# Optimization experiments

Hardware: AMD Instinct MI355X
Metric: run time of the kernel (lower is better)

Reference implementation:

```python
import jax, jax.numpy as jnp
import numpy as np

N, NFEAT, NHID, NCLASS, NHEADS = 4096, 512, 64, 16, 8
ALPHA = 0.2  # LeakyReLU negative slope


def setup_inputs() -> dict:
    key = jax.random.key(0)
    ks = jax.random.split(key, 5)
    return {
        "x": jax.random.normal(ks[0], (N, NFEAT), jnp.float32),
        "Wh": jax.random.normal(ks[1], (NHEADS, NFEAT, NHID), jnp.float32) * 0.05,
        "ah": jax.random.normal(ks[2], (NHEADS, 2 * NHID), jnp.float32) * 0.1,
        "Wo": jax.random.normal(ks[3], (NHEADS * NHID, NCLASS), jnp.float32) * 0.05,
        "ao": jax.random.normal(ks[4], (2 * NCLASS,), jnp.float32) * 0.1,
    }


def _gat_layer(x, W, a, concat):
    # h = x W  [N, F]
    h = x @ W
    F = h.shape[-1]
    # additive score decomposes: e_ij = leakyrelu(h_i . a[:F] + h_j . a[F:])
    s_src = h @ a[:F]  # [N]
    s_dst = h @ a[F:]  # [N]
    e = jax.nn.leaky_relu(s_src[:, None] + s_dst[None, :], ALPHA)  # [N, N]
    att = jax.nn.softmax(e, axis=1)
    feat = att @ h  # [N, F]
    return jax.nn.elu(feat) if concat else feat


def reference(x, Wh, ah, Wo, ao):
    # multi-head layers, concatenated along features (head-major order, as torch cat)
    heads = jax.vmap(lambda W, a: _gat_layer(x, W, a, True))(Wh, ah)  # [H, N, nhid]
    xc = jnp.transpose(heads, (1, 0, 2)).reshape(x.shape[0], -1)  # [N, H*nhid]
    out = jax.nn.elu(_gat_layer(xc, Wo, ao, False))  # [N, nclass]
    return jax.nn.log_softmax(out, axis=1)
```

## Files before the change

### kernel.cpp

```cpp
#include <hip/hip_runtime.h>
#include <math.h>

#define N 4096
#define NFEAT 512
#define NHID 64
#define NCLASS 16
#define NHEADS 8
#define ALPHA 0.2f
#define NC 256
#define JSPL 8
#define JLEN (N / JSPL)
#define HSTR 520

typedef __attribute__((ext_vector_type(8))) short bf16x8;
typedef __attribute__((ext_vector_type(4))) float f32x4;

__device__ inline unsigned short f2bf(float f) {
  unsigned u = __float_as_uint(f);
  unsigned r = u + 0x7fffu + ((u >> 16) & 1u);
  return (unsigned short)(r >> 16);
}
__device__ inline float bf2f(unsigned short u) {
  return __uint_as_float(((unsigned)u) << 16);
}
__device__ inline unsigned mono(float f) {
  unsigned u = __float_as_uint(f);
  return (u & 0x80000000u) ? ~u : (u | 0x80000000u);
}
__device__ inline float unmono(unsigned m) {
  return (m >> 31) ? __uint_as_float(m & 0x7FFFFFFFu) : __uint_as_float(~m);
}

__global__ __launch_bounds__(256) void k_pack(const float* __restrict__ x,
                                              const float* __restrict__ Wh,
                                              const float* __restrict__ Wo,
                                              unsigned short* __restrict__ xb,
                                              unsigned short* __restrict__ Wt,
                                              unsigned short* __restrict__ Wt2,
                                              unsigned* __restrict__ tmax2u) {
  int b = blockIdx.x;
  if (b < 2048) {
    int i = (b * 256 + threadIdx.x) * 4;
    float4 v = *(const float4*)(x + i);
    ushort4 o;
    o.x = f2bf(v.x); o.y = f2bf(v.y); o.z = f2bf(v.z); o.w = f2bf(v.w);
    *(ushort4*)(xb + i) = o;
  } else if (b < 2112) {
    int idx = b - 2048;
    int kt = idx & 7, hd = idx >> 3;
    __shared__ float ld[64][65];
    const float* src = Wh + ((size_t)hd * NFEAT + kt * 64) * NHID;
    int r = threadIdx.x >> 2, c0 = (threadIdx.x & 3) * 16;
#pragma unroll
    for (int j = 0; j < 4; ++j) {
      float4 v = *(const float4*)(src + (size_t)r * NHID + c0 + j * 4);
      ld[r][c0 + j * 4 + 0] = v.x; ld[r][c0 + j * 4 + 1] = v.y;
      ld[r][c0 + j * 4 + 2] = v.z; ld[r][c0 + j * 4 + 3] = v.w;
    }
    __syncthreads();
    int n = threadIdx.x >> 2, kq = threadIdx.x & 3;
    unsigned short tmp[16];
#pragma unroll
    for (int j = 0; j < 16; ++j) tmp[j] = f2bf(ld[kq * 16 + j][n]);
    unsigned short* dst = Wt + ((size_t)hd * 64 + n) * NFEAT + kt * 64 + kq * 16;
    ((uint4*)dst)[0] = *(uint4*)tmp;
    ((uint4*)dst)[1] = *(uint4*)(tmp + 8);
  } else {
    for (int e = threadIdx.x; e < NFEAT * NCLASS; e += 256) {
      int n = e & 15, k = e >> 4;
      Wt2[(size_t)n * NFEAT + k] = f2bf(Wo[(size_t)k * NCLASS + n]);
    }
    if (threadIdx.x == 0) *tmax2u = 0u;
  }
}

__global__ __launch_bounds__(256) void k_gemm_h(const unsigned short* __restrict__ xb,
                                                const unsigned short* __restrict__ Wt,
                                                const float* __restrict__ ah,
                                                unsigned short* __restrict__ h1b,
                                                float* __restrict__ ssrc,
                                                float* __restrict__ sdst) {
  const int hd = blockIdx.y;
  const int i0 = blockIdx.x * 128;
  const int t = threadIdx.x;
  const int w = t >> 6, lane = t & 63;
  const int lr = lane & 15, kg = lane >> 4;
  const int wm = (w & 1) * 64, wn = (w >> 1) * 32;
  __shared__ uint4 Als[128][4];
  __shared__ uint4 Bls[64][4];
  __shared__ float sredS[128][2];
  __shared__ float sredD[128][2];
  const unsigned short* xrow = xb + (size_t)i0 * NFEAT;
  const unsigned short* wrow = Wt + (size_t)hd * 64 * NFEAT;

  f32x4 acc[4][2];
#pragma unroll
  for (int a = 0; a < 4; ++a)
#pragma unroll
    for (int b = 0; b < 2; ++b) acc[a][b] = (f32x4){0.f, 0.f, 0.f, 0.f};

  const int u0 = t, u1 = t + 256;
  const int ra0 = u0 >> 2, sa0 = ((u0 & 3) ^ (ra0 & 3)) * 8;
  const int ra1 = u1 >> 2, sa1 = ((u1 & 3) ^ (ra1 & 3)) * 8;
  const int rb0 = t >> 2,  sb0 = ((t & 3) ^ (rb0 & 3)) * 8;
  const int wbase = t & ~63;

  for (int k0 = 0; k0 < NFEAT; k0 += 32) {
    __builtin_amdgcn_global_load_lds(
        (const __attribute__((address_space(1))) void*)(xrow + (size_t)ra0 * NFEAT + k0 + sa0),
        (__attribute__((address_space(3))) void*)((uint4*)Als + wbase), 16, 0, 0);
    __builtin_amdgcn_global_load_lds(
        (const __attribute__((address_space(1))) void*)(xrow + (size_t)ra1 * NFEAT + k0 + sa1),
        (__attribute__((address_space(3))) void*)((uint4*)Als + 256 + wbase), 16, 0, 0);
    __builtin_amdgcn_global_load_lds(
        (const __attribute__((address_space(1))) void*)(wrow + (size_t)rb0 * NFEAT + k0 + sb0),
        (__attribute__((address_space(3))) void*)((uint4*)Bls + wbase), 16, 0, 0);
    __syncthreads();
    bf16x8 af[4], bfv[2];
#pragma unroll
    for (int mb = 0; mb < 4; ++mb) {
      int row = wm + mb * 16 + lr;
      af[mb] = __builtin_bit_cast(bf16x8, Als[row][kg ^ (row & 3)]);
    }
#pragma unroll
    for (int nb = 0; nb < 2; ++nb) {
      int col = wn + nb * 16 + lr;
      bfv[nb] = __builtin_bit_cast(bf16x8, Bls[col][kg ^ (col & 3)]);
    }
#pragma unroll
    for (int mb = 0; mb < 4; ++mb)
#pragma unroll
      for (int nb = 0; nb < 2; ++nb)
        acc[mb][nb] = __builtin_amdgcn_mfma_f32_16x16x32_bf16(af[mb], bfv[nb], acc[mb][nb], 0, 0, 0);
    __syncthreads();
  }

  unsigned short* hout = h1b + ((size_t)hd * N + i0) * NHID;
#pragma unroll
  for (int mb = 0; mb < 4; ++mb)
#pragma unroll
    for (int nb = 0; nb < 2; ++nb) {
      int rbase = wm + mb * 16 + kg * 4;
      int col = wn + nb * 16 + lr;
#pragma unroll
      for (int reg = 0; reg < 4; ++reg)
        hout[(size_t)(rbase + reg) * NHID + col] = f2bf(acc[mb][nb][reg]);
    }

  float aS[2], aD[2];
#pragma unroll
  for (int nb = 0; nb < 2; ++nb) {
    aS[nb] = ah[hd * 128 + wn + nb * 16 + lr];
    aD[nb] = ah[hd * 128 + 64 + wn + nb * 16 + lr];
  }
#pragma unroll
  for (int mb = 0; mb < 4; ++mb)
#pragma unroll
    for (int reg = 0; reg < 4; ++reg) {
      float ps = acc[mb][0][reg] * aS[0] + acc[mb][1][reg] * aS[1];
      float pd = acc[mb][0][reg] * aD[0] + acc[mb][1][reg] * aD[1];
#pragma unroll
      for (int m = 1; m < 16; m <<= 1) { ps += __shfl_xor(ps, m); pd += __shfl_xor(pd, m); }
      if (lr == 0) {
        int rl = wm + mb * 16 + kg * 4 + reg;
        sredS[rl][w >> 1] = ps;
        sredD[rl][w >> 1] = pd;
      }
    }
  __syncthreads();
  if (t < 128) {
    ssrc[(size_t)hd * N + i0 + t] = sredS[t][0] + sredS[t][1];
    sdst[(size_t)hd * N + i0 + t] = sredD[t][0] + sredD[t][1];
  }
}

__global__ __launch_bounds__(256) void k_rank(const float* __restrict__ t,
                                              const float* __restrict__ ssrc,
                                              float* __restrict__ ts,
                                              int* __restrict__ perm,
                                              int* __restrict__ ksp) {
  int hd = blockIdx.y;
  const float* th = t + (size_t)hd * N;
  __shared__ unsigned skey[N];
  int tid = threadIdx.x;
  for (int i = tid; i < N; i += 256)
    skey[i] = (mono(th[i]) & 0xFFFFF000u) | (unsigned)i;
  __syncthreads();
  int wv = tid >> 6, lane = tid & 63;
  int jbase = blockIdx.x * 64 + wv * 16;
  unsigned kj[16], qk[16];
  int cnt[16], cq[16];
#pragma unroll
  for (int jj = 0; jj < 16; ++jj) {
    kj[jj] = skey[jbase + jj];
    qk[jj] = (mono(-ssrc[(size_t)hd * N + jbase + jj]) & 0xFFFFF000u) | 0xFFFu;
    cnt[jj] = 0; cq[jj] = 0;
  }
  for (int c = 0; c < N; c += 64) {
    unsigned key = skey[c + lane];
#pragma unroll
    for (int jj = 0; jj < 16; ++jj) {
      cnt[jj] += __popcll(__ballot(key < kj[jj]));
      cq[jj]  += __popcll(__ballot(key < qk[jj]));
    }
  }
  int myc = 0, myq = 0;
#pragma unroll
  for (int jj = 0; jj < 16; ++jj)
    if (lane == jj) { myc = cnt[jj]; myq = cq[jj]; }
  if (lane < 16) {
    int j = jbase + lane;
    ts[(size_t)hd * N + myc] = th[j];
    perm[(size_t)hd * N + myc] = j;
    ksp[(size_t)hd * N + j] = myq;
  }
}

__global__ __launch_bounds__(256) void k_chunksum1(const float* __restrict__ ts,
                                                   const int* __restrict__ perm,
                                                   const unsigned short* __restrict__ h1b,
                                                   float* __restrict__ csA,
                                                   float* __restrict__ csB,
                                                   float* __restrict__ csAz,
                                                   float* __restrict__ csBz) {
  int hd = blockIdx.y, lane = threadIdx.x & 63;
  int c = blockIdx.x * 4 + (threadIdx.x >> 6);
  int r0 = c * 16;
  float tm = ts[(size_t)hd * N + N - 1];
  float tvv = ts[(size_t)hd * N + r0 + (lane & 15)];
  float ev = expf((lane < 16 ? ALPHA : 1.f) * (tvv - tm));
  int pvv = perm[(size_t)hd * N + r0 + (lane & 15)];
  float sA = 0.f, sB = 0.f, zA = 0.f, zB = 0.f;
#pragma unroll
  for (int r = 0; r < 16; ++r) {
    float eA = __shfl(ev, r);
    float eB = __shfl(ev, 16 + r);
    int p = __shfl(pvv, r);
    float hv = bf2f(h1b[((size_t)hd * N + p) * NHID + lane]);
    sA += eA * hv; sB += eB * hv; zA += eA; zB += eB;
  }
  csA[((size_t)hd * NC + c) * NHID + lane] = sA;
  csB[((size_t)hd * NC + c) * NHID + lane] = sB;
  if (lane == 0) { csAz[hd * NC + c] = zA; csBz[hd * NC + c] = zB; }
}

__global__ __launch_bounds__(1024) void k_chunkscan1(float* __restrict__ csA,
                                                     float* __restrict__ csB,
                                                     float* __restrict__ csAz,
                                                     float* __restrict__ csBz) {
  int hd = blockIdx.x;
  int t = threadIdx.x, w = t >> 6, lane = t & 63;
  __shared__ float pA[16][64], pB[16][64];
  __shared__ float pAz[16], pBz[16];
  float rA[16], rB[16], rAz[16], rBz[16];
#pragma unroll
  for (int cc = 0; cc < 16; ++cc) {
    int c = w * 16 + cc;
    rA[cc] = csA[((size_t)hd * NC + c) * NHID + lane];
    rB[cc] = csB[((size_t)hd * NC + c) * NHID + lane];
    rAz[cc] = csAz[hd * NC + c];
    rBz[cc] = csBz[hd * NC + c];
  }
  float tA = 0.f, tB = 0.f, tAz = 0.f, tBz = 0.f;
#pragma unroll
  for (int cc = 0; cc < 16; ++cc) { tA += rA[cc]; tB += rB[cc]; tAz += rAz[cc]; tBz += rBz[cc]; }
  pA[w][lane] = tA; pB[w][lane] = tB;
  if (lane == 0) { pAz[w] = tAz; pBz[w] = tBz; }
  __syncthreads();
  float bA = 0.f, bAz = 0.f, bB = 0.f, bBz = 0.f;
  for (int w2 = 0; w2 < w; ++w2) { bA += pA[w2][lane]; bAz += pAz[w2]; }
  for (int w2 = w + 1; w2 < 16; ++w2) { bB += pB[w2][lane]; bBz += pBz[w2]; }
  float run = bA, runz = bAz;
#pragma unroll
  for (int cc = 0; cc < 16; ++cc) {
    int c = w * 16 + cc;
    csA[((size_t)hd * NC + c) * NHID + lane] = run; run += rA[cc];
    if (lane == 0) csAz[hd * NC + c] = runz;
    runz += rAz[cc];
  }
  run = bB; runz = bBz;
#pragma unroll
  for (int cc = 15; cc >= 0; --cc) {
    int c = w * 16 + cc;
    csB[((size_t)hd * NC + c) * NHID + lane] = run; run += rB[cc];
    if (lane == 0) csBz[hd * NC + c] = runz;
    runz += rBz[cc];
  }
}

__global__ __launch_bounds__(256) void k_combine1(const float* __restrict__ ssrc,
                                                  const float* __restrict__ ts,
                                                  const int* __restrict__ perm,
                                                  const int* __restrict__ ksp,
                                                  const unsigned short* __restrict__ h1b,
                                                  const float* __restrict__ csA,
                                                  const float* __restrict__ csB,
                                                  const float* __restrict__ csAz,
                                                  const float* __restrict__ csBz,
                                                  unsigned short* __restrict__ xcb) {
  int hd = blockIdx.x >> 8;
  int base = (blockIdx.x & 255) * 16;
  int w = threadIdx.x >> 6, lane = threadIdx.x & 63;
  const float* tsh = ts + (size_t)hd * N;
  float tm = tsh[N - 1];
  for (int it = 0; it < 4; ++it) {
    int i = base + w * 4 + it;
    float s = ssrc[(size_t)hd * N + i];
    int k = ksp[(size_t)hd * N + i];
    int c = k >> 4; if (c > NC - 1) c = NC - 1;
    int c0 = c * 16;
    float v = s + tm;
    float m = fmaxf(v, ALPHA * v);
    float wA = expf(ALPHA * v - m), wB = expf(v - m);
    size_t cb = (size_t)hd * NC + c;
    float numA = csA[cb * NHID + lane];
    float numB = csB[cb * NHID + lane];
    float zA = csAz[cb], zB = csBz[cb];
    int r15 = lane & 15;
    float tvv = tsh[c0 + r15];
    int pvv = perm[(size_t)hd * N + c0 + r15];
    float ev = expf(((c0 + r15) < k ? ALPHA : 1.f) * (tvv - tm));
#pragma unroll
    for (int r = 0; r < 16; ++r) {
      float e = __shfl(ev, r);
      int p = __shfl(pvv, r);
      float hv = bf2f(h1b[((size_t)hd * N + p) * NHID + lane]);
      bool isA = (c0 + r) < k;
      if (isA) { numA += e * hv; zA += e; } else { numB += e * hv; zB += e; }
    }
    float Z = wA * zA + wB * zB;
    float f = (wA * numA + wB * numB) / Z;
    float e2 = f > 0.f ? f : expf(f) - 1.f;
    xcb[(size_t)i * (NHEADS * NHID) + hd * NHID + lane] = f2bf(e2);
  }
}

__global__ __launch_bounds__(256) void k_gemm2(const unsigned short* __restrict__ xcb,
                                               const unsigned short* __restrict__ Wt2,
                                               const float* __restrict__ ao,
                                               unsigned short* __restrict__ h2b,
                                               float* __restrict__ ssrc,
                                               float* __restrict__ sdst,
                                               unsigned* __restrict__ tmax2u) {
  const int t = threadIdx.x;
  const int w = t >> 6, lane = t & 63;
  const int lr = lane & 15, kg = lane >> 4;
  const int i0 = blockIdx.x * 64 + w * 16;
  __shared__ float sd[64];
  f32x4 acc = (f32x4){0.f, 0.f, 0.f, 0.f};
  const unsigned short* arow = xcb + (size_t)(i0 + lr) * NFEAT;
  const unsigned short* brow = Wt2 + (size_t)lr * NFEAT;
#pragma unroll
  for (int k0 = 0; k0 < NFEAT; k0 += 32) {
    bf16x8 af = __builtin_bit_cast(bf16x8, *(const uint4*)(arow + k0 + kg * 8));
    bf16x8 bv = __builtin_bit_cast(bf16x8, *(const uint4*)(brow + k0 + kg * 8));
    acc = __builtin_amdgcn_mfma_f32_16x16x32_bf16(af, bv, acc, 0, 0, 0);
  }
  float aS = ao[lr], aD = ao[16 + lr];
#pragma unroll
  for (int reg = 0; reg < 4; ++reg) {
    int row = i0 + kg * 4 + reg;
    h2b[(size_t)row * NCLASS + lr] = f2bf(acc[reg]);
    float ps = acc[reg] * aS, pd = acc[reg] * aD;
#pragma unroll
    for (int m = 1; m < 16; m <<= 1) { ps += __shfl_xor(ps, m); pd += __shfl_xor(pd, m); }
    if (lr == 0) {
      ssrc[row] = ps;
      sdst[row] = pd;
      sd[w * 16 + kg * 4 + reg] = pd;
    }
  }
  __syncthreads();
  if (t < 64) {
    float v = sd[t];
#pragma unroll
    for (int m = 32; m; m >>= 1) v = fmaxf(v, __shfl_xor(v, m));
    if (t == 0) atomicMax(tmax2u, mono(v));
  }
}

__global__ __launch_bounds__(256) void k_attn2p(const float* __restrict__ ssrc,
                                                const float* __restrict__ t,
                                                const unsigned short* __restrict__ h2b,
                                                const unsigned* __restrict__ tmax2u,
                                                float* __restrict__ pnum,
                                                float* __restrict__ pz) {
  __shared__ float tl[JLEN];
  __shared__ unsigned short hsT[16 * HSTR];
  int tid = threadIdx.x;
  int jb = blockIdx.y;
  if (tid < 128) {
    int i4 = tid * 4;
    *(float4*)(tl + i4) = *(const float4*)(t + jb * JLEN + i4);
  }
#pragma unroll
  for (int rep = 0; rep < 2; ++rep) {
    int j = rep * 256 + tid;
    const uint4* src = (const uint4*)(h2b + (size_t)(jb * JLEN + j) * NCLASS);
    uint4 a = src[0], b = src[1];
    unsigned short v[16];
    *(uint4*)v = a; *(uint4*)(v + 8) = b;
#pragma unroll
    for (int c = 0; c < 16; ++c) hsT[c * HSTR + j] = v[c];
  }
  __syncthreads();
  int w = tid >> 6, lane = tid & 63;
  int lr = lane & 15, kg = lane >> 4;
  int ib = blockIdx.x * 64 + w * 16;
  float tmax = unmono(*tmax2u);
  float s = ssrc[ib + lr];
  float v0 = s + tmax;
  float rowm = fmaxf(v0, ALPHA * v0);
  f32x4 acc = (f32x4){0.f, 0.f, 0.f, 0.f};
  float zpart = 0.f;
#pragma unroll
  for (int c = 0; c < JLEN / 32; ++c) {
    const float* tp = tl + c * 32 + kg * 8;
    float e[8];
#pragma unroll
    for (int m = 0; m < 8; ++m) {
      float v = s + tp[m];
      e[m] = __expf(fmaxf(v, ALPHA * v) - rowm);
      zpart += e[m];
    }
    unsigned pk[4];
#pragma unroll
    for (int p = 0; p < 4; ++p)
      pk[p] = ((unsigned)f2bf(e[2 * p + 1]) << 16) | (unsigned)f2bf(e[2 * p]);
    bf16x8 af = __builtin_bit_cast(bf16x8, *(uint4*)pk);
    bf16x8 bf = __builtin_bit_cast(bf16x8,
        *(const uint4*)(hsT + lr * HSTR + c * 32 + kg * 8));
    acc = __builtin_amdgcn_mfma_f32_16x16x32_bf16(af, bf, acc, 0, 0, 0);
  }
  zpart += __shfl_xor(zpart, 16);
  zpart += __shfl_xor(zpart, 32);
#pragma unroll
  for (int reg = 0; reg < 4; ++reg)
    pnum[((size_t)jb * N + ib + kg * 4 + reg) * NCLASS + lr] = acc[reg];
  if (lane < 16) pz[(size_t)jb * N + ib + lane] = zpart;
}

__global__ __launch_bounds__(256) void k_attn2f(const float* __restrict__ pnum,
                                                const float* __restrict__ pz,
                                                float* __restrict__ out) {
  int g = threadIdx.x >> 4, cl = threadIdx.x & 15;
  int i = blockIdx.x * 16 + g;
  float nsum = 0.f, zsum = 0.f;
#pragma unroll
  for (int jb = 0; jb < JSPL; ++jb) {
    nsum += pnum[((size_t)jb * N + i) * NCLASS + cl];
    zsum += pz[(size_t)jb * N + i];
  }
  float o = nsum / zsum;
  o = o > 0.f ? o : expf(o) - 1.f;
  float mo = o;
#pragma unroll
  for (int mk = 1; mk < 16; mk <<= 1) mo = fmaxf(mo, __shfl_xor(mo, mk, 16));
  float sum = expf(o - mo);
#pragma unroll
  for (int mk = 1; mk < 16; mk <<= 1) sum += __shfl_xor(sum, mk, 16);
  out[(size_t)i * NCLASS + cl] = o - mo - logf(sum);
}

extern "C" void kernel_launch(void* const* d_in, const int* in_sizes, int n_in,
                              void* d_out, int out_size, void* d_ws, size_t ws_size,
                              hipStream_t stream) {
  const float* x  = (const float*)d_in[0];
  const float* Wh = (const float*)d_in[1];
  const float* ah = (const float*)d_in[2];
  const float* Wo = (const float*)d_in[3];
  const float* ao = (const float*)d_in[4];
  float* out = (float*)d_out;

  char* base = (char*)d_ws;
  size_t off = 0;
  auto alloc_f = [&](size_t n) -> float* {
    float* p = (float*)(base + off);
    off = (off + n * sizeof(float) + 255) & ~(size_t)255;
    return p;
  };
  auto alloc_i = [&](size_t n) -> int* {
    int* p = (int*)(base + off);
    off = (off + n * sizeof(int) + 255) & ~(size_t)255;
    return p;
  };
  auto alloc_u16 = [&](size_t n) -> unsigned short* {
    unsigned short* p = (unsigned short*)(base + off);
    off = (off + n * sizeof(unsigned short) + 255) & ~(size_t)255;
    return p;
  };

  unsigned short* xbf = alloc_u16((size_t)N * NFEAT);
  unsigned short* Wt  = alloc_u16((size_t)NHEADS * NHID * NFEAT);
  unsigned short* Wt2 = alloc_u16((size_t)NCLASS * NFEAT);
  unsigned short* h1b = alloc_u16((size_t)NHEADS * N * NHID);
  float* ssrc1 = alloc_f((size_t)NHEADS * N);
  float* sdst1 = alloc_f((size_t)NHEADS * N);
  float* ts1   = alloc_f((size_t)NHEADS * N);
  int*   perm1 = alloc_i((size_t)NHEADS * N);
  int*   ksp1  = alloc_i((size_t)NHEADS * N);
  float* csA1  = alloc_f((size_t)NHEADS * NC * NHID);
  float* csB1  = alloc_f((size_t)NHEADS * NC * NHID);
  float* csAz1 = alloc_f(NHEADS * NC);
  float* csBz1 = alloc_f(NHEADS * NC);
  unsigned short* xcb = alloc_u16((size_t)N * NHEADS * NHID);
  unsigned short* h2b = alloc_u16((size_t)N * NCLASS);
  float* ssrc2 = alloc_f(N);
  float* sdst2 = alloc_f(N);
  unsigned* tmax2u = (unsigned*)alloc_i(1);
  float* pnum  = alloc_f((size_t)JSPL * N * NCLASS);
  float* pz    = alloc_f((size_t)JSPL * N);

  if (off > ws_size) return;

  hipLaunchKernelGGL(k_pack, dim3(2113), dim3(256), 0, stream, x, Wh, Wo, xbf, Wt, Wt2, tmax2u);

  hipLaunchKernelGGL(k_gemm_h, dim3(N / 128, NHEADS), dim3(256), 0, stream, xbf, Wt, ah, h1b, ssrc1, sdst1);
  hipLaunchKernelGGL(k_rank, dim3(64, NHEADS), dim3(256), 0, stream, sdst1, ssrc1, ts1, perm1, ksp1);
  hipLaunchKernelGGL(k_chunksum1, dim3(64, NHEADS), dim3(256), 0, stream, ts1, perm1, h1b, csA1, csB1, csAz1, csBz1);
  hipLaunchKernelGGL(k_chunkscan1, dim3(NHEADS), dim3(1024), 0, stream, csA1, csB1, csAz1, csBz1);
  hipLaunchKernelGGL(k_combine1, dim3(NHEADS * 256), dim3(256), 0, stream, ssrc1, ts1, perm1, ksp1, h1b, csA1, csB1, csAz1, csBz1, xcb);

  hipLaunchKernelGGL(k_gemm2, dim3(N / 64), dim3(256), 0, stream, xcb, Wt2, ao, h2b, ssrc2, sdst2, tmax2u);
  hipLaunchKernelGGL(k_attn2p, dim3(N / 64, JSPL), dim3(256), 0, stream, ssrc2, sdst2, h2b, tmax2u, pnum, pz);
  hipLaunchKernelGGL(k_attn2f, dim3(N / 16), dim3(256), 0, stream, pnum, pz, out);
}
```

Before: 105.7 us.

## Replace sort-based layer-1 attention with dense MFMA attention over transposed h

Drops the rank/sort, chunk-sum, chunk-scan and combine pipeline for the first GAT layer. In its place is a single dense attention kernel: it uses a per-head global max of the destination scores (found with atomicMax in the projection GEMM) as the softmax shift, builds exp weights as bf16 and multiplies them against h with MFMA. h is now stored transposed so tiles stage into LDS with contiguous loads. This cuts four launches and the gather-heavy sorted traversal, but the attention becomes O(N^2·F) matrix work per head and the exp weights are rounded to bf16.

After: 106.0 us. About the same (+0.3%).

```diff
diff --git a/kernel.cpp b/kernel.cpp
--- a/kernel.cpp
+++ b/kernel.cpp
@@ -7,10 +7,11 @@
 #define NCLASS 16
 #define NHEADS 8
 #define ALPHA 0.2f
-#define NC 256
 #define JSPL 8
 #define JLEN (N / JSPL)
 #define HSTR 520
+#define J1 256
+#define H1STR 264
 
 typedef __attribute__((ext_vector_type(8))) short bf16x8;
 typedef __attribute__((ext_vector_type(4))) float f32x4;
@@ -19,9 +20,6 @@
   unsigned u = __float_as_uint(f);
   unsigned r = u + 0x7fffu + ((u >> 16) & 1u);
   return (unsigned short)(r >> 16);
-}
-__device__ inline float bf2f(unsigned short u) {
-  return __uint_as_float(((unsigned)u) << 16);
 }
 __device__ inline unsigned mono(float f) {
   unsigned u = __float_as_uint(f);
@@ -37,6 +35,7 @@
                                               unsigned short* __restrict__ xb,
                                               unsigned short* __restrict__ Wt,
                                               unsigned short* __restrict__ Wt2,
+                                              unsigned* __restrict__ tmax1u,
                                               unsigned* __restrict__ tmax2u) {
   int b = blockIdx.x;
   if (b < 2048) {
@@ -70,6 +69,7 @@
       int n = e & 15, k = e >> 4;
       Wt2[(size_t)n * NFEAT + k] = f2bf(Wo[(size_t)k * NCLASS + n]);
     }
+    if (threadIdx.x < NHEADS) tmax1u[threadIdx.x] = 0u;
     if (threadIdx.x == 0) *tmax2u = 0u;
   }
 }
@@ -77,9 +77,10 @@
 __global__ __launch_bounds__(256) void k_gemm_h(const unsigned short* __restrict__ xb,
                                                 const unsigned short* __restrict__ Wt,
                                                 const float* __restrict__ ah,
-                                                unsigned short* __restrict__ h1b,
+                                                unsigned short* __restrict__ h1T,
                                                 float* __restrict__ ssrc,
-                                                float* __restrict__ sdst) {
+                                                float* __restrict__ sdst,
+                                                unsigned* __restrict__ tmax1u) {
   const int hd = blockIdx.y;
   const int i0 = blockIdx.x * 128;
   const int t = threadIdx.x;
@@ -135,16 +136,17 @@
     __syncthreads();
   }
 
-  unsigned short* hout = h1b + ((size_t)hd * N + i0) * NHID;
+  unsigned short* hT = h1T + (size_t)hd * NHID * N;
 #pragma unroll
   for (int mb = 0; mb < 4; ++mb)
 #pragma unroll
     for (int nb = 0; nb < 2; ++nb) {
-      int rbase = wm + mb * 16 + kg * 4;
       int col = wn + nb * 16 + lr;
-#pragma unroll
-      for (int reg = 0; reg < 4; ++reg)
-        hout[(size_t)(rbase + reg) * NHID + col] = f2bf(acc[mb][nb][reg]);
+      int rbase = i0 + wm + mb * 16 + kg * 4;
+      ushort4 o;
+      o.x = f2bf(acc[mb][nb][0]); o.y = f2bf(acc[mb][nb][1]);
+      o.z = f2bf(acc[mb][nb][2]); o.w = f2bf(acc[mb][nb][3]);
+      *(ushort4*)(hT + (size_t)col * N + rbase) = o;
     }
 
   float aS[2], aD[2];
@@ -169,169 +171,85 @@
     }
   __syncthreads();
   if (t < 128) {
-    ssrc[(size_t)hd * N + i0 + t] = sredS[t][0] + sredS[t][1];
-    sdst[(size_t)hd * N + i0 + t] = sredD[t][0] + sredD[t][1];
-  }
-}
-
-__global__ __launch_bounds__(256) void k_rank(const float* __restrict__ t,
-                                              const float* __restrict__ ssrc,
-                                              float* __restrict__ ts,
-                                              int* __restrict__ perm,
-                                              int* __restrict__ ksp) {
-  int hd = blockIdx.y;
-  const float* th = t + (size_t)hd * N;
-  __shared__ unsigned skey[N];
-  int tid = threadIdx.x;
-  for (int i = tid; i < N; i += 256)
-    skey[i] = (mono(th[i]) & 0xFFFFF000u) | (unsigned)i;
-  __syncthreads();
-  int wv = tid >> 6, lane = tid & 63;
-  int jbase = blockIdx.x * 64 + wv * 16;
-  unsigned kj[16], qk[16];
-  int cnt[16], cq[16];
-#pragma unroll
-  for (int jj = 0; jj < 16; ++jj) {
-    kj[jj] = skey[jbase + jj];
-    qk[jj] = (mono(-ssrc[(size_t)hd * N + jbase + jj]) & 0xFFFFF000u) | 0xFFFu;
-    cnt[jj] = 0; cq[jj] = 0;
-  }
-  for (int c = 0; c < N; c += 64) {
-    unsigned key = skey[c + lane];
-#pragma unroll
-    for (int jj = 0; jj < 16; ++jj) {
-      cnt[jj] += __popcll(__ballot(key < kj[jj]));
-      cq[jj]  += __popcll(__ballot(key < qk[jj]));
-    }
-  }
-  int myc = 0, myq = 0;
-#pragma unroll
-  for (int jj = 0; jj < 16; ++jj)
-    if (lane == jj) { myc = cnt[jj]; myq = cq[jj]; }
-  if (lane < 16) {
-    int j = jbase + lane;
-    ts[(size_t)hd * N + myc] = th[j];
-    perm[(size_t)hd * N + myc] = j;
-    ksp[(size_t)hd * N + j] = myq;
-  }
-}
-
-__global__ __launch_bounds__(256) void k_chunksum1(const float* __restrict__ ts,
-                                                   const int* __restrict__ perm,
-                                                   const unsigned short* __restrict__ h1b,
-                                                   float* __restrict__ csA,
-                                                   float* __restrict__ csB,
-                                                   float* __restrict__ csAz,
-                                                   float* __restrict__ csBz) {
-  int hd = blockIdx.y, lane = threadIdx.x & 63;
-  int c = blockIdx.x * 4 + (threadIdx.x >> 6);
-  int r0 = c * 16;
-  float tm = ts[(size_t)hd * N + N - 1];
-  float tvv = ts[(size_t)hd * N + r0 + (lane & 15)];
-  float ev = expf((lane < 16 ? ALPHA : 1.f) * (tvv - tm));
-  int pvv = perm[(size_t)hd * N + r0 + (lane & 15)];
-  float sA = 0.f, sB = 0.f, zA = 0.f, zB = 0.f;
-#pragma unroll
-  for (int r = 0; r < 16; ++r) {
-    float eA = __shfl(ev, r);
-    float eB = __shfl(ev, 16 + r);
-    int p = __shfl(pvv, r);
-    float hv = bf2f(h1b[((size_t)hd * N + p) * NHID + lane]);
-    sA += eA * hv; sB += eB * hv; zA += eA; zB += eB;
-  }
-  csA[((size_t)hd * NC + c) * NHID + lane] = sA;
-  csB[((size_t)hd * NC + c) * NHID + lane] = sB;
-  if (lane == 0) { csAz[hd * NC + c] = zA; csBz[hd * NC + c] = zB; }
-}
-
-__global__ __launch_bounds__(1024) void k_chunkscan1(float* __restrict__ csA,
-                                                     float* __restrict__ csB,
-                                                     float* __restrict__ csAz,
-                                                     float* __restrict__ csBz) {
-  int hd = blockIdx.x;
-  int t = threadIdx.x, w = t >> 6, lane = t & 63;
-  __shared__ float pA[16][64], pB[16][64];
-  __shared__ float pAz[16], pBz[16];
-  float rA[16], rB[16], rAz[16], rBz[16];
-#pragma unroll
-  for (int cc = 0; cc < 16; ++cc) {
-    int c = w * 16 + cc;
-    rA[cc] = csA[((size_t)hd * NC + c) * NHID + lane];
-    rB[cc] = csB[((size_t)hd * NC + c) * NHID + lane];
-    rAz[cc] = csAz[hd * NC + c];
-    rBz[cc] = csBz[hd * NC + c];
-  }
-  float tA = 0.f, tB = 0.f, tAz = 0.f, tBz = 0.f;
-#pragma unroll
-  for (int cc = 0; cc < 16; ++cc) { tA += rA[cc]; tB += rB[cc]; tAz += rAz[cc]; tBz += rBz[cc]; }
-  pA[w][lane] = tA; pB[w][lane] = tB;
-  if (lane == 0) { pAz[w] = tAz; pBz[w] = tBz; }
-  __syncthreads();
-  float bA = 0.f, bAz = 0.f, bB = 0.f, bBz = 0.f;
-  for (int w2 = 0; w2 < w; ++w2) { bA += pA[w2][lane]; bAz += pAz[w2]; }
-  for (int w2 = w + 1; w2 < 16; ++w2) { bB += pB[w2][lane]; bBz += pBz[w2]; }
-  float run = bA, runz = bAz;
-#pragma unroll
-  for (int cc = 0; cc < 16; ++cc) {
-    int c = w * 16 + cc;
-    csA[((size_t)hd * NC + c) * NHID + lane] = run; run += rA[cc];
-    if (lane == 0) csAz[hd * NC + c] = runz;
-    runz += rAz[cc];
-  }
-  run = bB; runz = bBz;
-#pragma unroll
-  for (int cc = 15; cc >= 0; --cc) {
-    int c = w * 16 + cc;
-    csB[((size_t)hd * NC + c) * NHID + lane] = run; run += rB[cc];
-    if (lane == 0) csBz[hd * NC + c] = runz;
-    runz += rBz[cc];
-  }
-}
-
-__global__ __launch_bounds__(256) void k_combine1(const float* __restrict__ ssrc,
-                                                  const float* __restrict__ ts,
-                                                  const int* __restrict__ perm,
-                                                  const int* __restrict__ ksp,
-                                                  const unsigned short* __restrict__ h1b,
-                                                  const float* __restrict__ csA,
-                                                  const float* __restrict__ csB,
-                                                  const float* __restrict__ csAz,
-                                                  const float* __restrict__ csBz,
-                                                  unsigned short* __restrict__ xcb) {
-  int hd = blockIdx.x >> 8;
-  int base = (blockIdx.x & 255) * 16;
-  int w = threadIdx.x >> 6, lane = threadIdx.x & 63;
-  const float* tsh = ts + (size_t)hd * N;
-  float tm = tsh[N - 1];
-  for (int it = 0; it < 4; ++it) {
-    int i = base + w * 4 + it;
-    float s = ssrc[(size_t)hd * N + i];
-    int k = ksp[(size_t)hd * N + i];
-    int c = k >> 4; if (c > NC - 1) c = NC - 1;
-    int c0 = c * 16;
-    float v = s + tm;
-    float m = fmaxf(v, ALPHA * v);
-    float wA = expf(ALPHA * v - m), wB = expf(v - m);
-    size_t cb = (size_t)hd * NC + c;
-    float numA = csA[cb * NHID + lane];
-    float numB = csB[cb * NHID + lane];
-    float zA = csAz[cb], zB = csBz[cb];
-    int r15 = lane & 15;
-    float tvv = tsh[c0 + r15];
-    int pvv = perm[(size_t)hd * N + c0 + r15];
-    float ev = expf(((c0 + r15) < k ? ALPHA : 1.f) * (tvv - tm));
-#pragma unroll
-    for (int r = 0; r < 16; ++r) {
-      float e = __shfl(ev, r);
-      int p = __shfl(pvv, r);
-      float hv = bf2f(h1b[((size_t)hd * N + p) * NHID + lane]);
-      bool isA = (c0 + r) < k;
-      if (isA) { numA += e * hv; zA += e; } else { numB += e * hv; zB += e; }
-    }
-    float Z = wA * zA + wB * zB;
-    float f = (wA * numA + wB * numB) / Z;
-    float e2 = f > 0.f ? f : expf(f) - 1.f;
-    xcb[(size_t)i * (NHEADS * NHID) + hd * NHID + lane] = f2bf(e2);
+    float vs = sredS[t][0] + sredS[t][1];
+    float vd = sredD[t][0] + sredD[t][1];
+    ssrc[(size_t)hd * N + i0 + t] = vs;
+    sdst[(size_t)hd * N + i0 + t] = vd;
+    float m = vd;
+#pragma unroll
+    for (int mk = 32; mk; mk >>= 1) m = fmaxf(m, __shfl_xor(m, mk));
+    if ((t & 63) == 0) atomicMax(tmax1u + hd, mono(m));
+  }
+}
+
+__global__ __launch_bounds__(256) void k_attn1(const float* __restrict__ ssrc,
+                                               const float* __restrict__ sdst,
+                                               const unsigned short* __restrict__ h1T,
+                                               const unsigned* __restrict__ tmax1u,
+                                               unsigned short* __restrict__ xcb) {
+  __shared__ float tl[J1];
+  __shared__ unsigned short hsT[64 * H1STR];
+  const int hd = blockIdx.y;
+  const int tid = threadIdx.x, w = tid >> 6, lane = tid & 63;
+  const int lr = lane & 15, kg = lane >> 4;
+  const int row16 = blockIdx.x * 64 + w * 16;
+  const unsigned short* hTh = h1T + (size_t)hd * NHID * N;
+  const float* th = sdst + (size_t)hd * N;
+  float tmax = unmono(tmax1u[hd]);
+  float s = ssrc[(size_t)hd * N + row16 + lr];
+  float v0 = s + tmax;
+  float rowm = fmaxf(v0, ALPHA * v0);
+  f32x4 acc[4];
+#pragma unroll
+  for (int nb = 0; nb < 4; ++nb) acc[nb] = (f32x4){0.f, 0.f, 0.f, 0.f};
+  float zpart = 0.f;
+
+  for (int jc = 0; jc < N / J1; ++jc) {
+    if (tid < 64) *(float4*)(tl + tid * 4) = *(const float4*)(th + jc * J1 + tid * 4);
+#pragma unroll
+    for (int rep = 0; rep < 8; ++rep) {
+      int u = rep * 256 + tid;
+      int r = u >> 5, cu = u & 31;
+      *(uint4*)(hsT + r * H1STR + cu * 8) =
+          *(const uint4*)(hTh + (size_t)r * N + jc * J1 + cu * 8);
+    }
+    __syncthreads();
+#pragma unroll
+    for (int c = 0; c < J1 / 32; ++c) {
+      const float* tp = tl + c * 32 + kg * 8;
+      float e[8];
+#pragma unroll
+      for (int m = 0; m < 8; ++m) {
+        float v = s + tp[m];
+        e[m] = __expf(fmaxf(v, ALPHA * v) - rowm);
+        zpart += e[m];
+      }
+      unsigned pk[4];
+#pragma unroll
+      for (int p = 0; p < 4; ++p)
+        pk[p] = ((unsigned)f2bf(e[2 * p + 1]) << 16) | (unsigned)f2bf(e[2 * p]);
+      bf16x8 af = __builtin_bit_cast(bf16x8, *(uint4*)pk);
+#pragma unroll
+      for (int nb = 0; nb < 4; ++nb) {
+        bf16x8 bf = __builtin_bit_cast(bf16x8,
+            *(const uint4*)(hsT + (nb * 16 + lr) * H1STR + c * 32 + kg * 8));
+        acc[nb] = __builtin_amdgcn_mfma_f32_16x16x32_bf16(af, bf, acc[nb], 0, 0, 0);
+      }
+    }
+    __syncthreads();
+  }
+  zpart += __shfl_xor(zpart, 16);
+  zpart += __shfl_xor(zpart, 32);
+#pragma unroll
+  for (int reg = 0; reg < 4; ++reg) {
+    float rz = 1.f / __shfl(zpart, kg * 4 + reg);
+    int row = row16 + kg * 4 + reg;
+#pragma unroll
+    for (int nb = 0; nb < 4; ++nb) {
+      float f = acc[nb][reg] * rz;
+      float e2 = f > 0.f ? f : expf(f) - 1.f;
+      xcb[(size_t)row * (NHEADS * NHID) + hd * NHID + nb * 16 + lr] = f2bf(e2);
+    }
   }
 }
 
@@ -493,16 +411,10 @@
   unsigned short* xbf = alloc_u16((size_t)N * NFEAT);
   unsigned short* Wt  = alloc_u16((size_t)NHEADS * NHID * NFEAT);
   unsigned short* Wt2 = alloc_u16((size_t)NCLASS * NFEAT);
-  unsigned short* h1b = alloc_u16((size_t)NHEADS * N * NHID);
+  unsigned short* h1T = alloc_u16((size_t)NHEADS * NHID * N);
   float* ssrc1 = alloc_f((size_t)NHEADS * N);
   float* sdst1 = alloc_f((size_t)NHEADS * N);
-  float* ts1   = alloc_f((size_t)NHEADS * N);
-  int*   perm1 = alloc_i((size_t)NHEADS * N);
-  int*   ksp1  = alloc_i((size_t)NHEADS * N);
-  float* csA1  = alloc_f((size_t)NHEADS * NC * NHID);
-  float* csB1  = alloc_f((size_t)NHEADS * NC * NHID);
-  float* csAz1 = alloc_f(NHEADS * NC);
-  float* csBz1 = alloc_f(NHEADS * NC);
+  unsigned* tmax1u = (unsigned*)alloc_i(NHEADS);
   unsigned short* xcb = alloc_u16((size_t)N * NHEADS * NHID);
   unsigned short* h2b = alloc_u16((size_t)N * NCLASS);
   float* ssrc2 = alloc_f(N);
@@ -513,13 +425,10 @@
 
   if (off > ws_size) return;
 
-  hipLaunchKernelGGL(k_pack, dim3(2113), dim3(256), 0, stream, x, Wh, Wo, xbf, Wt, Wt2, tmax2u);
-
-  hipLaunchKernelGGL(k_gemm_h, dim3(N / 128, NHEADS), dim3(256), 0, stream, xbf, Wt, ah, h1b, ssrc1, sdst1);
-  hipLaunchKernelGGL(k_rank, dim3(64, NHEADS), dim3(256), 0, stream, sdst1, ssrc1, ts1, perm1, ksp1);
-  hipLaunchKernelGGL(k_chunksum1, dim3(64, NHEADS), dim3(256), 0, stream, ts1, perm1, h1b, csA1, csB1, csAz1, csBz1);
-  hipLaunchKernelGGL(k_chunkscan1, dim3(NHEADS), dim3(1024), 0, stream, csA1, csB1, csAz1, csBz1);
-  hipLaunchKernelGGL(k_combine1, dim3(NHEADS * 256), dim3(256), 0, stream, ssrc1, ts1, perm1, ksp1, h1b, csA1, csB1, csAz1, csBz1, xcb);
+  hipLaunchKernelGGL(k_pack, dim3(2113), dim3(256), 0, stream, x, Wh, Wo, xbf, Wt, Wt2, tmax1u, tmax2u);
+
+  hipLaunchKernelGGL(k_gemm_h, dim3(N / 128, NHEADS), dim3(256), 0, stream, xbf, Wt, ah, h1T, ssrc1, sdst1, tmax1u);
+  hipLaunchKernelGGL(k_attn1, dim3(N / 64, NHEADS), dim3(256), 0, stream, ssrc1, sdst1, h1T, tmax1u, xcb);
 
   hipLaunchKernelGGL(k_gemm2, dim3(N / 64), dim3(256), 0, stream, xcb, Wt2, ao, h2b, ssrc2, sdst2, tmax2u);
   hipLaunchKernelGGL(k_attn2p, dim3(N / 64, JSPL), dim3(256), 0, stream, ssrc2, sdst2, h2b, tmax2u, pnum, pz);
```
